# Performance work log

Hardware: AMD Instinct MI355X
Metric: run time of the kernel (lower is better)

Reference implementation:

```python
import jax, jax.numpy as jnp
import numpy as np
import math

B, T, C_EMB, H, M, P = 4, 8192, 1024, 16, 64, 8
D = C_EMB // H
L = int(math.log2(T // M)) - 1  # = 6 levels of coarse attention
SCALE_ATTN = True
NEG = -1e30


def setup_inputs() -> dict:
    key = jax.random.key(0)
    ks = jax.random.split(key, 4)
    x = jax.random.normal(ks[0], (B, T, C_EMB), jnp.float32)
    W_attn = jax.random.normal(ks[1], (C_EMB, 3 * C_EMB), jnp.float32) * (1.0 / math.sqrt(C_EMB))
    b_attn = jnp.zeros((3 * C_EMB,), jnp.float32)
    W_proj = jax.random.normal(ks[2], (C_EMB, C_EMB), jnp.float32) * (1.0 / math.sqrt(C_EMB))
    b_proj = jnp.zeros((C_EMB,), jnp.float32)
    return {"x": x, "W_attn": W_attn, "b_attn": b_attn, "W_proj": W_proj, "b_proj": b_proj}


def _shift(t, s):
    # shift blocks forward along axis 1 by s, zero-padding at the front
    pad = jnp.zeros_like(t[:, :s])
    return jnp.concatenate([pad, t[:, :-s]], axis=1)


def _fma_attention(q, k, v):
    # q, k, v: [BH, T, D]; q already scaled by 1/sqrt(D)
    BH = q.shape[0]
    # --- convolute(): avgpool downsampled K, V at each level ---
    Kls, Vls = [k], [v]
    for l in range(L):
        r = (M * 2 ** l) // P  # pool kernel = stride
        Kls.append(k.reshape(BH, T // r, r, D).mean(axis=2))
        Vls.append(v.reshape(BH, T // r, r, D).mean(axis=2))
    # --- stage1: banded QK at every level ---
    As = []
    # fine level 0: causal sliding window of M keys (j in [i-M+1, i])
    nb0 = T // M
    qb = q.reshape(BH, nb0, M, D)
    kb = k.reshape(BH, nb0, M, D)
    s_prev = jnp.einsum('bgqd,bgkd->bgqk', qb, _shift(kb, 1))
    s_self = jnp.einsum('bgqd,bgkd->bgqk', qb, kb)
    r_idx = jnp.arange(M)[:, None]
    c_idx = jnp.arange(M)[None, :]
    g_ok = (jnp.arange(nb0) >= 1)[None, :, None, None]
    s_prev = jnp.where((c_idx > r_idx) & g_ok, s_prev, NEG)
    s_self = jnp.where(c_idx <= r_idx, s_self, NEG)
    As.append(jnp.concatenate([s_prev, s_self], axis=-1).reshape(BH, T, 2 * M))
    # coarse levels l=1..L: query block (width w) attends to the P summaries of
    # each of the two preceding coarse blocks (causal, left-to-right)
    for l in range(1, L + 1):
        w = M * 2 ** (l - 1)
        nb = T // w
        qw = q.reshape(BH, nb, w, D)
        kc = Kls[l].reshape(BH, nb, P, D)
        scores = []
        for s in (2, 1):
            sc = jnp.einsum('bgqd,bgpd->bgqp', qw, _shift(kc, s))
            ok = (jnp.arange(nb) >= s)[None, :, None, None]
            scores.append(jnp.where(ok, sc, NEG))
        As.append(jnp.concatenate(scores, axis=-1).reshape(BH, T, 2 * P))
    # --- fused multi-level softmax (shared max + shared normalizer) ---
    gmax = jnp.max(jnp.stack([a.max(axis=-1) for a in As], axis=-1), axis=-1)  # [BH, T]
    Es = [jnp.exp(a - gmax[..., None]) for a in As]
    scales = [1] + [((M * 2 ** (l - 1)) // P if SCALE_ATTN else 1) for l in range(1, L + 1)]
    denom = sum(float(s) * e.sum(axis=-1) for s, e in zip(scales, Es))[..., None]
    Cs = [float(s) * e / denom for s, e in zip(scales, Es)]
    # --- stage2: banded CV ---
    vb = v.reshape(BH, nb0, M, D)
    C0 = Cs[0].reshape(BH, nb0, M, 2 * M)
    out = (jnp.einsum('bgqk,bgkd->bgqd', C0[..., :M], _shift(vb, 1)) +
           jnp.einsum('bgqk,bgkd->bgqd', C0[..., M:], vb)).reshape(BH, T, D)
    for l in range(1, L + 1):
        w = M * 2 ** (l - 1)
        nb = T // w
        vc = Vls[l].reshape(BH, nb, P, D)
        Cl = Cs[l].reshape(BH, nb, w, 2 * P)
        ol = (jnp.einsum('bgqp,bgpd->bgqd', Cl[..., :P], _shift(vc, 2)) +
              jnp.einsum('bgqp,bgpd->bgqd', Cl[..., P:], _shift(vc, 1)))
        out = out + ol.reshape(BH, T, D)
    return out


def reference(x, W_attn, b_attn, W_proj, b_proj):
    Bx, Tx, Cx = x.shape
    qkv = x @ W_attn + b_attn
    q, k, v = jnp.split(qkv, 3, axis=-1)

    def heads(t):
        return t.reshape(Bx, Tx, H, D).transpose(0, 2, 1, 3).reshape(Bx * H, Tx, D)

    q = heads(q) / math.sqrt(D)
    o = _fma_attention(q, heads(k), heads(v))
    o = o.reshape(Bx, H, Tx, D).transpose(0, 2, 1, 3).reshape(Bx, Tx, Cx)
    return o @ W_proj + b_proj
```

## Files before the change

### kernel.cpp

```cpp
#include <hip/hip_runtime.h>
#include <hip/hip_bf16.h>
#include <stdint.h>


typedef float  f32x4  __attribute__((ext_vector_type(4)));
typedef __bf16 bf16x8 __attribute__((ext_vector_type(8)));
typedef unsigned short ushort8 __attribute__((ext_vector_type(8)));
typedef unsigned short ushort4v __attribute__((ext_vector_type(4)));

__device__ __forceinline__ unsigned short f2bf(float f) {
  union { float f; unsigned u; } v; v.f = f;
  unsigned r = v.u + 0x7fffu + ((v.u >> 16) & 1u);
  return (unsigned short)(r >> 16);
}
__device__ __forceinline__ float bf2f(unsigned short s) {
  union { unsigned u; float f; } v; v.u = ((unsigned)s) << 16;
  return v.f;
}
__device__ __forceinline__ bf16x8 ld_bf8(const unsigned short* p) {
  return __builtin_bit_cast(bf16x8, *(const ushort8*)p);
}
__device__ __forceinline__ f32x4 mfma16(bf16x8 a, bf16x8 b, f32x4 c) {
  return __builtin_amdgcn_mfma_f32_16x16x32_bf16(a, b, c, 0, 0, 0);
}
__device__ __forceinline__ f32x4 zero4() {
  f32x4 z; z[0] = 0.f; z[1] = 0.f; z[2] = 0.f; z[3] = 0.f; return z;
}
__device__ __forceinline__ void gload16(const void* g, void* lds) {
  __builtin_amdgcn_global_load_lds(
      (const __attribute__((address_space(1))) void*)(uintptr_t)g,
      (__attribute__((address_space(3))) void*)(unsigned int)(uintptr_t)lds,
      16, 0, 0);
}

#define T_SEQ 8192
#define NPOOL 2016

#define SCHED0() __builtin_amdgcn_sched_barrier(0)
#define VMC(n)                                           \
  do {                                                   \
    SCHED0();                                            \
    asm volatile("s_waitcnt vmcnt(" #n ")" ::: "memory");\
    SCHED0();                                            \
  } while (0)

__global__ __launch_bounds__(256) void castx_k(const float* __restrict__ x,
                                               unsigned short* __restrict__ xb) {
  size_t i = ((size_t)blockIdx.x * 256 + threadIdx.x) * 8;
  float4 a = *(const float4*)(x + i);
  float4 b = *(const float4*)(x + i + 4);
  ushort8 o;
  o[0] = f2bf(a.x); o[1] = f2bf(a.y); o[2] = f2bf(a.z); o[3] = f2bf(a.w);
  o[4] = f2bf(b.x); o[5] = f2bf(b.y); o[6] = f2bf(b.z); o[7] = f2bf(b.w);
  *(ushort8*)(xb + i) = o;
}

__global__ __launch_bounds__(256) void transposeW_k(const float* __restrict__ w,
                                                    unsigned short* __restrict__ wt,
                                                    int R, int C) {
  __shared__ float tile[64 * 65];
  int cc = blockIdx.x, rc = blockIdx.y;
  int tid = threadIdx.x;
#pragma unroll
  for (int p = 0; p < 4; ++p) {
    int ci = p * 256 + tid;
    int r = ci >> 4, q4 = ci & 15;
    float4 v = *(const float4*)(w + (size_t)(rc * 64 + r) * C + cc * 64 + q4 * 4);
    tile[r * 65 + q4 * 4 + 0] = v.x;
    tile[r * 65 + q4 * 4 + 1] = v.y;
    tile[r * 65 + q4 * 4 + 2] = v.z;
    tile[r * 65 + q4 * 4 + 3] = v.w;
  }
  __syncthreads();
#pragma unroll
  for (int p = 0; p < 2; ++p) {
    int orow = p * 32 + (tid >> 3), tg = tid & 7;
    ushort8 ov;
#pragma unroll
    for (int i = 0; i < 8; ++i) ov[i] = f2bf(tile[(tg * 8 + i) * 65 + orow]);
    *(ushort8*)(wt + (size_t)(cc * 64 + orow) * R + rc * 64 + tg * 8) = ov;
  }
}

template<int NTILE_N, int EPI>
__global__ __launch_bounds__(512, 2) void gemm256(
    const unsigned short* __restrict__ A, const unsigned short* __restrict__ Bt,
    const float* __restrict__ bias,
    unsigned short* __restrict__ o0, unsigned short* __restrict__ o1,
    unsigned short* __restrict__ o2, float* __restrict__ fout) {
  extern __shared__ __align__(16) char smem[];
  const int K = 1024;
  const int nwg = 128 * NTILE_N;
  const int q = nwg >> 3;
  const int wg = ((int)blockIdx.x & 7) * q + ((int)blockIdx.x >> 3);
  const int tm = wg & 127, tn = wg >> 7;
  const int tid = threadIdx.x;
  const int wid = tid >> 6, lane = tid & 63;
  const int wm = wid >> 2, wn = wid & 3;
  const int lr = lane & 15, lg = lane >> 4;

  const int srow = tid >> 2;
  const int sseg = (tid & 3) ^ ((tid >> 3) & 3);
  const unsigned short* aSrc = A + (size_t)(tm * 256 + srow) * K + sseg * 8;
  const unsigned short* bSrc = Bt + (size_t)(tn * 256 + srow) * K + sseg * 8;
  const unsigned ldsT = (unsigned)tid * 16;

  const unsigned psel = (unsigned)((lg ^ ((lr >> 1) & 3)) * 16);
  const unsigned aBase = (unsigned)(wm * 8192 + lr * 64) + psel;
  const unsigned bBase = (unsigned)(16384 + wn * 4096 + lr * 64) + psel;

  f32x4 acc[8][4];
#pragma unroll
  for (int i = 0; i < 8; ++i)
#pragma unroll
    for (int j = 0; j < 4; ++j) acc[i][j] = zero4();

  bf16x8 rA0[4], rA1[4], rB0[4], rB1[4];

  auto SB = [&]() {
    SCHED0();
    __builtin_amdgcn_s_barrier();
    SCHED0();
  };
  auto stage2 = [&](int coffShorts, unsigned slotB) {
#pragma unroll
    for (int pass = 0; pass < 2; ++pass) {
      gload16(aSrc + (size_t)pass * 128 * K + coffShorts,
              smem + slotB + pass * 8192 + ldsT);
      gload16(bSrc + (size_t)pass * 128 * K + coffShorts,
              smem + slotB + 16384 + pass * 8192 + ldsT);
    }
  };
  auto rdA = [&](bf16x8 (&dst)[4], unsigned slotB, int ih) {
    const char* p = smem + slotB + aBase + ih * 4096;
#pragma unroll
    for (int ii = 0; ii < 4; ++ii)
      dst[ii] = ld_bf8((const unsigned short*)(p + ii * 1024));
  };
  auto rdB = [&](bf16x8 (&dst)[4], unsigned slotB) {
    const char* p = smem + slotB + bBase;
#pragma unroll
    for (int j = 0; j < 4; ++j)
      dst[j] = ld_bf8((const unsigned short*)(p + j * 1024));
  };
  auto cluster = [&](int rb, bf16x8 (&a)[4], bf16x8 (&b)[4]) {
    __builtin_amdgcn_s_setprio(1);
#pragma unroll
    for (int ii = 0; ii < 4; ++ii)
#pragma unroll
      for (int j = 0; j < 4; ++j)
        acc[rb + ii][j] = mfma16(b[j], a[ii], acc[rb + ii][j]);
    __builtin_amdgcn_s_setprio(0);
  };

  stage2(0, 0u);
  stage2(32, 32768u);
  stage2(64, 65536u);
  stage2(96, 98304u);
  VMC(12);
  SB();
  rdA(rA0, 0u, 0);
  rdB(rB0, 0u);

  for (int t = 0; t < 16; ++t) {
    const unsigned s0  = (unsigned)((2 * t) & 3) * 32768u;
    const unsigned s1  = (unsigned)((2 * t + 1) & 3) * 32768u;
    const unsigned sn0 = (unsigned)((2 * t + 2) & 3) * 32768u;
    rdA(rA1, s0, 1);
    if (t < 15) { VMC(8); } else { VMC(0); }
    SB();
    cluster(0, rA0, rB0);
    if (t < 14) stage2((t + 2) * 64, s0);
    rdA(rA0, s1, 0);
    rdB(rB1, s1);
    SB();
    cluster(4, rA1, rB0);
    rdA(rA1, s1, 1);
    if (t < 14) { VMC(8); } else if (t == 14) { VMC(4); }
    SB();
    cluster(0, rA0, rB1);
    if (t < 14) stage2((t + 2) * 64 + 32, s1);
    if (t < 15) { rdA(rA0, sn0, 0); rdB(rB0, sn0); }
    SB();
    cluster(4, rA1, rB1);
  }

  const int mBase = tm * 256 + wm * 128;
  const int nBase = tn * 256 + wn * 64;
  if (EPI == 0) {
    const int region = nBase >> 10, nn = nBase & 1023, hh = nn >> 6;
    unsigned short* dst = region == 0 ? o0 : (region == 1 ? o1 : o2);
#pragma unroll
    for (int j = 0; j < 4; ++j) {
      const int d0 = (nn & 63) + j * 16 + lg * 4;
      const float4 bv = *(const float4*)(bias + nBase + j * 16 + lg * 4);
#pragma unroll
      for (int i = 0; i < 8; ++i) {
        const int m = mBase + i * 16 + lr;
        const int bb = m >> 13, tq = m & 8191;
        ushort4v pk;
        pk[0] = f2bf(acc[i][j][0] + bv.x);
        pk[1] = f2bf(acc[i][j][1] + bv.y);
        pk[2] = f2bf(acc[i][j][2] + bv.z);
        pk[3] = f2bf(acc[i][j][3] + bv.w);
        *(ushort4v*)(dst + (((size_t)(bb * 16 + hh)) * T_SEQ + tq) * 64 + d0) = pk;
      }
    }
  } else {
#pragma unroll
    for (int j = 0; j < 4; ++j) {
      const int n0 = nBase + j * 16 + lg * 4;
      const float4 bv = *(const float4*)(bias + n0);
#pragma unroll
      for (int i = 0; i < 8; ++i) {
        const int m = mBase + i * 16 + lr;
        float4 ov;
        ov.x = acc[i][j][0] + bv.x;
        ov.y = acc[i][j][1] + bv.y;
        ov.z = acc[i][j][2] + bv.z;
        ov.w = acc[i][j][3] + bv.w;
        *(float4*)(fout + (size_t)m * 1024 + n0) = ov;
      }
    }
  }
}

__global__ __launch_bounds__(256) void transposeV_k(const unsigned short* __restrict__ v,
                                                    unsigned short* __restrict__ vt) {
  __shared__ float tile[64 * 65];
  int tc = blockIdx.x, bh = blockIdx.y;
  int tid = threadIdx.x;
#pragma unroll
  for (int p = 0; p < 2; ++p) {
    int r = p * 32 + (tid >> 3), cg = tid & 7;
    ushort8 u = *(const ushort8*)(v + ((size_t)bh * T_SEQ + (size_t)tc * 64 + r) * 64 + cg * 8);
#pragma unroll
    for (int i = 0; i < 8; ++i) tile[r * 65 + cg * 8 + i] = bf2f(u[i]);
  }
  __syncthreads();
#pragma unroll
  for (int p = 0; p < 2; ++p) {
    int dd = p * 32 + (tid >> 3), tg = tid & 7;
    ushort8 ov;
#pragma unroll
    for (int i = 0; i < 8; ++i) ov[i] = f2bf(tile[(tg * 8 + i) * 65 + dd]);
    *(ushort8*)(vt + ((size_t)bh * 64 + dd) * T_SEQ + (size_t)tc * 64 + tg * 8) = ov;
  }
}

__global__ __launch_bounds__(256) void poolK_k(const unsigned short* __restrict__ kin,
                                               unsigned short* __restrict__ kpool) {
  __shared__ float buf[64 * 65];
  int chunk = blockIdx.x, bh = blockIdx.y;
  int tid = threadIdx.x;
  int cg = tid & 7, orow = tid >> 3;
  float s[8];
#pragma unroll
  for (int i = 0; i < 8; ++i) s[i] = 0.f;
  const unsigned short* base =
      kin + ((size_t)bh * T_SEQ + chunk * 256 + orow * 8) * 64 + cg * 8;
#pragma unroll
  for (int rr = 0; rr < 8; ++rr) {
    ushort8 v = *(const ushort8*)(base + (size_t)rr * 64);
#pragma unroll
    for (int i = 0; i < 8; ++i) s[i] += bf2f(v[i]);
  }
  unsigned short* kp = kpool + (size_t)bh * NPOOL * 64;
  {
    ushort8 ov;
#pragma unroll
    for (int i = 0; i < 8; ++i) {
      s[i] *= 0.125f;
      ov[i] = f2bf(s[i]);
      buf[orow * 65 + cg * 8 + i] = s[i];
    }
    *(ushort8*)(kp + ((size_t)(chunk * 32 + orow)) * 64 + cg * 8) = ov;
  }
  __syncthreads();
  int srcR = 0, dstR = 32;
#pragma unroll
  for (int lvl = 2; lvl <= 6; ++lvl) {
    int rows = 32 >> (lvl - 1);
    int off = 2048 - (2048 >> (lvl - 1));
    if (orow < rows) {
      ushort8 ov;
      float tv[8];
#pragma unroll
      for (int i = 0; i < 8; ++i) {
        tv[i] = 0.5f * (buf[(srcR + 2 * orow) * 65 + cg * 8 + i] +
                        buf[(srcR + 2 * orow + 1) * 65 + cg * 8 + i]);
        ov[i] = f2bf(tv[i]);
      }
      *(ushort8*)(kp + ((size_t)(off + chunk * rows + orow)) * 64 + cg * 8) = ov;
#pragma unroll
      for (int i = 0; i < 8; ++i) buf[(dstR + orow) * 65 + cg * 8 + i] = tv[i];
    }
    __syncthreads();
    srcR = dstR;
    dstR += rows;
  }
}

__global__ __launch_bounds__(256) void poolV_k(const unsigned short* __restrict__ vt,
                                               unsigned short* __restrict__ vtpool) {
  __shared__ float buf[1024 + 512 + 256 + 128 + 64];
  int d = blockIdx.x, bh = blockIdx.y;
  int tid = threadIdx.x;
  const unsigned short* src = vt + ((size_t)bh * 64 + d) * T_SEQ;
  unsigned short* dst = vtpool + ((size_t)bh * 64 + d) * NPOOL;
#pragma unroll
  for (int p = 0; p < 4; ++p) {
    int oi = p * 256 + tid;
    ushort8 v = *(const ushort8*)(src + (size_t)oi * 8);
    float s = 0.f;
#pragma unroll
    for (int i = 0; i < 8; ++i) s += bf2f(v[i]);
    s *= 0.125f;
    dst[oi] = f2bf(s);
    buf[oi] = s;
  }
  __syncthreads();
  float* b1 = buf; float* b2 = buf + 1024;
#pragma unroll
  for (int p = 0; p < 2; ++p) {
    int oi = p * 256 + tid;
    float s = 0.5f * (b1[2 * oi] + b1[2 * oi + 1]);
    dst[1024 + oi] = f2bf(s);
    b2[oi] = s;
  }
  __syncthreads();
  float* b3 = b2 + 512;
  {
    float s = 0.5f * (b2[2 * tid] + b2[2 * tid + 1]);
    dst[1536 + tid] = f2bf(s);
    b3[tid] = s;
  }
  __syncthreads();
  float* b4 = b3 + 256;
  if (tid < 128) {
    float s = 0.5f * (b3[2 * tid] + b3[2 * tid + 1]);
    dst[1792 + tid] = f2bf(s);
    b4[tid] = s;
  }
  __syncthreads();
  float* b5 = b4 + 128;
  if (tid < 64) {
    float s = 0.5f * (b4[2 * tid] + b4[2 * tid + 1]);
    dst[1920 + tid] = f2bf(s);
    b5[tid] = s;
  }
  __syncthreads();
  if (tid < 32) {
    float s = 0.5f * (b5[2 * tid] + b5[2 * tid + 1]);
    dst[1984 + tid] = f2bf(s);
  }
}

__global__ __launch_bounds__(256) void attn_k(const unsigned short* __restrict__ q,
                                              const unsigned short* __restrict__ k,
                                              const unsigned short* __restrict__ kpool,
                                              const unsigned short* __restrict__ vt,
                                              const unsigned short* __restrict__ vtpool,
                                              unsigned short* __restrict__ o) {
  const int g = blockIdx.x;
  const int bh = blockIdx.y;
  const int tid = threadIdx.x;
  const int w = tid >> 6, l = tid & 63;
  const int lr = l & 15, lg = l >> 4;
  __shared__ unsigned short KV[224 * 64];
  __shared__ unsigned short Pl[64 * 264];

  const size_t qoff = ((size_t)bh * T_SEQ + (size_t)g * 64 + w * 16 + lr) * 64 + lg * 8;
  bf16x8 aq0 = ld_bf8(q + qoff);
  bf16x8 aq1 = ld_bf8(q + qoff + 32);
  SCHED0();

  const int krow = tid >> 3;
  const int kseg = tid & 7;
#pragma unroll
  for (int p = 0; p < 7; ++p) {
    const int row = p * 32 + krow;
    const unsigned short* src;
    if (row < 128) {
      int t0 = (g - 1) * 64 + row;
      if (t0 < 0) t0 = 0;
      src = k + ((size_t)bh * T_SEQ + t0) * 64;
    } else {
      const int pr = row - 128;
      const int lvl0 = pr >> 4;
      const int off = 2048 - (2048 >> lvl0);
      const int gl = g >> lvl0;
      int st = (gl - 2) * 8 + (pr & 15);
      if (st < 0) st = 0;
      src = kpool + ((size_t)bh * NPOOL + off + st) * 64;
    }
    gload16(src + (kseg ^ (row & 7)) * 8,
            ((char*)KV) + p * 4096 + (unsigned)tid * 16);
  }
  SCHED0();

  const int vr = tid >> 2;
  const int vg = tid & 3;
  const int vswz = vg ^ ((vr >> 1) & 3);
  ushort8 vstg[7];
#pragma unroll
  for (int s = 0; s < 7; ++s) {
    const int colsh = s * 32 + vswz * 8;
    const unsigned short* src;
    if (colsh < 128) {
      int t0 = (g - 1) * 64 + colsh;
      if (t0 < 0) t0 = 0;
      src = vt + ((size_t)bh * 64 + vr) * T_SEQ + t0;
    } else {
      const int c = colsh - 128;
      const int lvl = c >> 4;
      const int off = 2048 - (2048 >> lvl);
      const int gl = g >> lvl;
      int start = (gl - 2) * 8 + (c & 15);
      if (start < 0) start = 0;
      src = vtpool + ((size_t)bh * 64 + vr) * NPOOL + off + start;
    }
    vstg[s] = *(const ushort8*)src;
  }
  SCHED0();
  asm volatile("s_waitcnt vmcnt(7)" ::: "memory");
  SCHED0();
  __builtin_amdgcn_s_barrier();
  SCHED0();

  f32x4 S[14];
#pragma unroll
  for (int ct = 0; ct < 14; ++ct) S[ct] = zero4();
#pragma unroll
  for (int ct = 0; ct < 14; ++ct) {
    const int row = ct * 16 + lr;
    const unsigned short* kr = KV + row * 64;
    const int sw = row & 7;
    S[ct] = mfma16(aq0, ld_bf8(kr + (lg ^ sw) * 8), S[ct]);
    S[ct] = mfma16(aq1, ld_bf8(kr + ((lg + 4) ^ sw) * 8), S[ct]);
  }
  SCHED0();
  __builtin_amdgcn_s_barrier();
  SCHED0();

  const float NEGF = -1e30f;
#pragma unroll
  for (int ct = 0; ct < 14; ++ct) {
#pragma unroll
    for (int e = 0; e < 4; ++e) {
      int rr = w * 16 + lg * 4 + e;
      float s = S[ct][e] * 0.125f;
      bool valid;
      if (ct < 8) {
        int cc = ct * 16 + lr;
        valid = (cc > rr) && (cc <= rr + 64) && ((g >= 1) || (cc >= 64));
      } else {
        int lvl = ct - 7;
        int gl = g >> (lvl - 1);
        valid = gl >= ((lr < 8) ? 2 : 1);
      }
      S[ct][e] = valid ? s : NEGF;
    }
  }
  float mrow[4], invd[4];
#pragma unroll
  for (int e = 0; e < 4; ++e) {
    float mx = S[0][e];
#pragma unroll
    for (int ct = 1; ct < 14; ++ct) mx = fmaxf(mx, S[ct][e]);
    mx = fmaxf(mx, __shfl_xor(mx, 1));
    mx = fmaxf(mx, __shfl_xor(mx, 2));
    mx = fmaxf(mx, __shfl_xor(mx, 4));
    mx = fmaxf(mx, __shfl_xor(mx, 8));
    mrow[e] = mx;
  }
#pragma unroll
  for (int e = 0; e < 4; ++e) {
    float sum = 0.f;
#pragma unroll
    for (int ct = 0; ct < 14; ++ct) {
      float sc = (ct < 8) ? 1.0f : (float)(8 << (ct - 8));
      float ev = sc * __expf(S[ct][e] - mrow[e]);
      S[ct][e] = ev;
      sum += ev;
    }
    sum += __shfl_xor(sum, 1);
    sum += __shfl_xor(sum, 2);
    sum += __shfl_xor(sum, 4);
    sum += __shfl_xor(sum, 8);
    invd[e] = 1.0f / sum;
  }
#pragma unroll
  for (int ct = 0; ct < 14; ++ct) {
#pragma unroll
    for (int e = 0; e < 4; ++e) {
      int rr = w * 16 + lg * 4 + e;
      Pl[rr * 264 + ct * 16 + lr] = f2bf(S[ct][e] * invd[e]);
    }
  }
#pragma unroll
  for (int s = 0; s < 7; ++s)
    *(ushort8*)&KV[s * 2048 + vr * 32 + vg * 8] = vstg[s];
  __syncthreads();

  f32x4 O[4];
#pragma unroll
  for (int c2 = 0; c2 < 4; ++c2) O[c2] = zero4();
#pragma unroll
  for (int kc = 0; kc < 7; ++kc) {
    bf16x8 pa = ld_bf8(&Pl[(w * 16 + lr) * 264 + kc * 32 + lg * 8]);
#pragma unroll
    for (int c2 = 0; c2 < 4; ++c2) {
      const int row = c2 * 16 + lr;
      bf16x8 vb = ld_bf8(&KV[kc * 2048 + row * 32 + ((lg ^ ((lr >> 1) & 3)) * 8)]);
      O[c2] = mfma16(pa, vb, O[c2]);
    }
  }
  const int bb = bh >> 4, hh = bh & 15;
#pragma unroll
  for (int c2 = 0; c2 < 4; ++c2) {
    int d = c2 * 16 + lr;
#pragma unroll
    for (int e = 0; e < 4; ++e) {
      int t = g * 64 + w * 16 + lg * 4 + e;
      o[((size_t)bb * T_SEQ + t) * 1024 + hh * 64 + d] = f2bf(O[c2][e]);
    }
  }
}

extern "C" void kernel_launch(void* const* d_in, const int* in_sizes, int n_in,
                              void* d_out, int out_size, void* d_ws, size_t ws_size,
                              hipStream_t stream) {
  const float* x  = (const float*)d_in[0];
  const float* Wa = (const float*)d_in[1];
  const float* ba = (const float*)d_in[2];
  const float* Wp = (const float*)d_in[3];
  const float* bp = (const float*)d_in[4];
  float* out = (float*)d_out;
  char* ws = (char*)d_ws;
  const size_t MB = 1024 * 1024;

  unsigned short* xb  = (unsigned short*)(ws);
  unsigned short* qb  = (unsigned short*)(ws + 64 * MB);
  unsigned short* kb  = (unsigned short*)(ws + 128 * MB);
  unsigned short* vb  = (unsigned short*)(ws + 192 * MB);
  unsigned short* vt  = (unsigned short*)(ws + 256 * MB);
  unsigned short* wat = (unsigned short*)(ws + 320 * MB);
  unsigned short* wpt = (unsigned short*)(ws + 326 * MB);
  unsigned short* kpool  = xb;
  unsigned short* vtpool = (unsigned short*)(ws + 32 * MB);

  hipFuncSetAttribute((const void*)gemm256<12, 0>,
                      hipFuncAttributeMaxDynamicSharedMemorySize, 131072);
  hipFuncSetAttribute((const void*)gemm256<4, 1>,
                      hipFuncAttributeMaxDynamicSharedMemorySize, 131072);

  castx_k<<<16384, 256, 0, stream>>>(x, xb);
  transposeW_k<<<dim3(48, 16), 256, 0, stream>>>(Wa, wat, 1024, 3072);
  transposeW_k<<<dim3(16, 16), 256, 0, stream>>>(Wp, wpt, 1024, 1024);
  gemm256<12, 0><<<1536, 512, 131072, stream>>>(xb, wat, ba, qb, kb, vb, nullptr);
  transposeV_k<<<dim3(128, 64), 256, 0, stream>>>(vb, vt);
  poolK_k<<<dim3(32, 64), 256, 0, stream>>>(kb, kpool);
  poolV_k<<<dim3(64, 64), 256, 0, stream>>>(vt, vtpool);
  attn_k<<<dim3(128, 64), 256, 0, stream>>>(qb, kb, kpool, vt, vtpool, vb);
  gemm256<4, 1><<<512, 512, 131072, stream>>>(vb, wpt, bp, nullptr, nullptr, nullptr, out);
}
```

Baseline: 536.7 us.

## Keep softmax probabilities in registers via transposed QK MFMA and lane shuffles

Swaps the MFMA operand order for QK so each lane holds a single query row's scores. The row max and sum then reduce mostly within a thread, with only two cross-lane shuffles. The probabilities are packed to bf16 with v_cvt_pk_bf16_f32 and redistributed into the PV A-operand layout using __shfl, which removes the Pl shared-memory buffer and its scattered 2-byte stores. This cuts LDS traffic and LDS footprint, which may also raise occupancy, at the cost of many ds_bpermute shuffles and extra selects.

```diff
diff --git a/kernel.cpp b/kernel.cpp
--- a/kernel.cpp
+++ b/kernel.cpp
@@ -7,6 +7,7 @@
 typedef __bf16 bf16x8 __attribute__((ext_vector_type(8)));
 typedef unsigned short ushort8 __attribute__((ext_vector_type(8)));
 typedef unsigned short ushort4v __attribute__((ext_vector_type(4)));
+typedef unsigned uint4v __attribute__((ext_vector_type(4)));
 
 __device__ __forceinline__ unsigned short f2bf(float f) {
   union { float f; unsigned u; } v; v.f = f;
@@ -368,7 +369,6 @@
   const int w = tid >> 6, l = tid & 63;
   const int lr = l & 15, lg = l >> 4;
   __shared__ unsigned short KV[224 * 64];
-  __shared__ unsigned short Pl[64 * 264];
 
   const size_t qoff = ((size_t)bh * T_SEQ + (size_t)g * 64 + w * 16 + lr) * 64 + lg * 8;
   bf16x8 aq0 = ld_bf8(q + qoff);
@@ -436,71 +436,88 @@
     const int row = ct * 16 + lr;
     const unsigned short* kr = KV + row * 64;
     const int sw = row & 7;
-    S[ct] = mfma16(aq0, ld_bf8(kr + (lg ^ sw) * 8), S[ct]);
-    S[ct] = mfma16(aq1, ld_bf8(kr + ((lg + 4) ^ sw) * 8), S[ct]);
+    S[ct] = mfma16(ld_bf8(kr + (lg ^ sw) * 8), aq0, S[ct]);
+    S[ct] = mfma16(ld_bf8(kr + ((lg + 4) ^ sw) * 8), aq1, S[ct]);
   }
   SCHED0();
   __builtin_amdgcn_s_barrier();
   SCHED0();
 
+#pragma unroll
+  for (int s = 0; s < 7; ++s)
+    *(ushort8*)&KV[s * 2048 + vr * 32 + vg * 8] = vstg[s];
+
   const float NEGF = -1e30f;
+  const int qq = w * 16 + lr;
 #pragma unroll
   for (int ct = 0; ct < 14; ++ct) {
 #pragma unroll
     for (int e = 0; e < 4; ++e) {
-      int rr = w * 16 + lg * 4 + e;
       float s = S[ct][e] * 0.125f;
       bool valid;
       if (ct < 8) {
-        int cc = ct * 16 + lr;
-        valid = (cc > rr) && (cc <= rr + 64) && ((g >= 1) || (cc >= 64));
+        int kk = ct * 16 + lg * 4 + e;
+        valid = (kk > qq) && (kk <= qq + 64) && ((g >= 1) || (kk >= 64));
       } else {
         int lvl = ct - 7;
         int gl = g >> (lvl - 1);
-        valid = gl >= ((lr < 8) ? 2 : 1);
+        valid = gl >= ((lg < 2) ? 2 : 1);
       }
       S[ct][e] = valid ? s : NEGF;
     }
   }
-  float mrow[4], invd[4];
-#pragma unroll
-  for (int e = 0; e < 4; ++e) {
-    float mx = S[0][e];
-#pragma unroll
-    for (int ct = 1; ct < 14; ++ct) mx = fmaxf(mx, S[ct][e]);
-    mx = fmaxf(mx, __shfl_xor(mx, 1));
-    mx = fmaxf(mx, __shfl_xor(mx, 2));
-    mx = fmaxf(mx, __shfl_xor(mx, 4));
-    mx = fmaxf(mx, __shfl_xor(mx, 8));
-    mrow[e] = mx;
-  }
-#pragma unroll
-  for (int e = 0; e < 4; ++e) {
-    float sum = 0.f;
-#pragma unroll
-    for (int ct = 0; ct < 14; ++ct) {
-      float sc = (ct < 8) ? 1.0f : (float)(8 << (ct - 8));
-      float ev = sc * __expf(S[ct][e] - mrow[e]);
+  float mx = S[0][0];
+#pragma unroll
+  for (int ct = 0; ct < 14; ++ct)
+#pragma unroll
+    for (int e = 0; e < 4; ++e) mx = fmaxf(mx, S[ct][e]);
+  mx = fmaxf(mx, __shfl_xor(mx, 16));
+  mx = fmaxf(mx, __shfl_xor(mx, 32));
+  float sum = 0.f;
+#pragma unroll
+  for (int ct = 0; ct < 14; ++ct) {
+    const float sc = (ct < 8) ? 1.0f : (float)(8 << (ct - 8));
+#pragma unroll
+    for (int e = 0; e < 4; ++e) {
+      float ev = sc * __expf(S[ct][e] - mx);
       S[ct][e] = ev;
       sum += ev;
     }
-    sum += __shfl_xor(sum, 1);
-    sum += __shfl_xor(sum, 2);
-    sum += __shfl_xor(sum, 4);
-    sum += __shfl_xor(sum, 8);
-    invd[e] = 1.0f / sum;
-  }
+  }
+  sum += __shfl_xor(sum, 16);
+  sum += __shfl_xor(sum, 32);
+  const float invd = 1.0f / sum;
+
+  unsigned pw[14][2];
 #pragma unroll
   for (int ct = 0; ct < 14; ++ct) {
-#pragma unroll
-    for (int e = 0; e < 4; ++e) {
-      int rr = w * 16 + lg * 4 + e;
-      Pl[rr * 264 + ct * 16 + lr] = f2bf(S[ct][e] * invd[e]);
-    }
-  }
-#pragma unroll
-  for (int s = 0; s < 7; ++s)
-    *(ushort8*)&KV[s * 2048 + vr * 32 + vg * 8] = vstg[s];
+    float p0 = S[ct][0] * invd, p1 = S[ct][1] * invd;
+    float p2 = S[ct][2] * invd, p3 = S[ct][3] * invd;
+    asm("v_cvt_pk_bf16_f32 %0, %1, %2" : "=v"(pw[ct][0]) : "v"(p0), "v"(p1));
+    asm("v_cvt_pk_bf16_f32 %0, %1, %2" : "=v"(pw[ct][1]) : "v"(p2), "v"(p3));
+  }
+
+  const int src0 = lr + ((lg & 1) << 5);
+  const int src1 = src0 + 16;
+  const bool odd = (lg & 2) != 0;
+  bf16x8 paf[7];
+#pragma unroll
+  for (int kc = 0; kc < 7; ++kc) {
+    unsigned we0 = __shfl((int)pw[2 * kc][0], src0);
+    unsigned we1 = __shfl((int)pw[2 * kc][1], src0);
+    unsigned we2 = __shfl((int)pw[2 * kc][0], src1);
+    unsigned we3 = __shfl((int)pw[2 * kc][1], src1);
+    unsigned wo0 = __shfl((int)pw[2 * kc + 1][0], src0);
+    unsigned wo1 = __shfl((int)pw[2 * kc + 1][1], src0);
+    unsigned wo2 = __shfl((int)pw[2 * kc + 1][0], src1);
+    unsigned wo3 = __shfl((int)pw[2 * kc + 1][1], src1);
+    uint4v fw;
+    fw[0] = odd ? wo0 : we0;
+    fw[1] = odd ? wo1 : we1;
+    fw[2] = odd ? wo2 : we2;
+    fw[3] = odd ? wo3 : we3;
+    paf[kc] = __builtin_bit_cast(bf16x8, fw);
+  }
   __syncthreads();
 
   f32x4 O[4];
@@ -508,12 +525,11 @@
   for (int c2 = 0; c2 < 4; ++c2) O[c2] = zero4();
 #pragma unroll
   for (int kc = 0; kc < 7; ++kc) {
-    bf16x8 pa = ld_bf8(&Pl[(w * 16 + lr) * 264 + kc * 32 + lg * 8]);
 #pragma unroll
     for (int c2 = 0; c2 < 4; ++c2) {
       const int row = c2 * 16 + lr;
       bf16x8 vb = ld_bf8(&KV[kc * 2048 + row * 32 + ((lg ^ ((lr >> 1) & 3)) * 8)]);
-      O[c2] = mfma16(pa, vb, O[c2]);
+      O[c2] = mfma16(paf[kc], vb, O[c2]);
     }
   }
   const int bb = bh >> 4, hh = bh & 15;
```

After: 506.3 us. 5.7% less time.
